# Kernel tuning notes

Hardware: AMD Instinct MI355X
Metric: run time of the kernel (lower is better)

The kernel has to match this reference:

```python
import jax, jax.numpy as jnp
import numpy as np

N = 100_000   # nodes
E = 1_600_000 # directed edges
G = 2048      # graphs in batch
NF = 78       # input node features
DIM = 32      # GIN hidden dim
L = 5         # num GIN layers
OUT = 128     # output_dim
BN_EPS = 1e-5


def setup_inputs() -> dict:
    key = jax.random.key(0)
    ks = jax.random.split(key, 8)
    s = 0.1
    return {
        "x": jax.random.normal(ks[0], (N, NF), jnp.float32),
        "edge_index": jax.random.randint(ks[1], (2, E), 0, N, jnp.int32),
        "batch": jnp.sort(jax.random.randint(ks[2], (N,), 0, G, jnp.int32)),
        "W1_0": (jax.random.normal(ks[3], (NF, DIM), jnp.float32) * s),
        "W1_rest": (jax.random.normal(ks[4], (L - 1, DIM, DIM), jnp.float32) * s),
        "b1": jnp.zeros((L, DIM), jnp.float32),
        "W2": (jax.random.normal(ks[5], (L, DIM, DIM), jnp.float32) * s),
        "b2": jnp.zeros((L, DIM), jnp.float32),
        "gamma": jnp.ones((L, DIM), jnp.float32),
        "beta": jnp.zeros((L, DIM), jnp.float32),
        "Wfc": (jax.random.normal(ks[6], (DIM, OUT), jnp.float32) * s),
        "bfc": jnp.zeros((OUT,), jnp.float32),
    }


def reference(x, edge_index, batch, W1_0, W1_rest, b1, W2, b2, gamma, beta, Wfc, bfc):
    src, dst = edge_index[0], edge_index[1]
    h = x
    for i in range(L):
        # GINConv (eps=0): h_i' = MLP(h_i + sum_{j->i} h_j)
        agg = jax.ops.segment_sum(h[src], dst, num_segments=N)  # [N, d]
        h = h + agg
        W1 = W1_0 if i == 0 else W1_rest[i - 1]
        h = jnp.maximum(h @ W1 + b1[i], 0.0) @ W2[i] + b2[i]
        # ReLU then BatchNorm1d (training mode: batch stats, biased var)
        h = jnp.maximum(h, 0.0)
        mu = h.mean(axis=0)
        var = h.var(axis=0)
        h = gamma[i] * (h - mu) * jax.lax.rsqrt(var + BN_EPS) + beta[i]
    pooled = jax.ops.segment_sum(h, batch, num_segments=G)  # global_add_pool [G, DIM]
    return jnp.maximum(pooled @ Wfc + bfc, 0.0)  # dropout is identity (eval)
```

## Files before the change

kernel.cpp:

```cpp
#include <hip/hip_runtime.h>
#include <hip/hip_fp16.h>

#define N_NODES 100000
#define N_EDGES 1600000
#define N_GRAPHS 2048
#define NFEAT 78
#define DIM 32
#define NLAYERS 5
#define OUTD 128
#define BN_EPS 1e-5f
#define NPB 32
#define NT (N_NODES / NPB)
#define NB2 ((NT + 1) / 2)
#define NBUK 391
#define BNODES 256
#define STRIDE 4608
#define EPB 4096
#define NBLK ((N_EDGES + EPB - 1) / EPB)
#define NSLOT 16
#define PSTRIDE (NSLOT * 2 * DIM)
#define OSTR (BNODES + 1)
#define WIN 4096
#define NWIN ((N_NODES + WIN - 1) / WIN)

__device__ __forceinline__ float2 up2(unsigned u) {
    __half2 h = *reinterpret_cast<__half2*>(&u);
    return __half22float2(h);
}
__device__ __forceinline__ unsigned pk2(float a, float b) {
    __half2 h = __floats2half2_rn(a, b);
    return *reinterpret_cast<unsigned*>(&h);
}

__global__ __launch_bounds__(256) void prep_kernel(
    const int* __restrict__ ei, int* __restrict__ bcnt, int* __restrict__ bdata,
    const float* __restrict__ x, const float* __restrict__ W1_0,
    unsigned short* __restrict__ y)
{
    __shared__ int cur[NBUK];
    __shared__ int gbl[NBUK];
    __shared__ float Wl[NFEAT * DIM];
    int tid = threadIdx.x;

    if (blockIdx.x < NBLK) {
        int base = blockIdx.x * EPB;
        for (int i = tid; i < NBUK; i += 256) cur[i] = 0;
        __syncthreads();

        int ew[16], eb[16];
        const int4* s4 = (const int4*)ei;
        const int4* d4 = (const int4*)(ei + N_EDGES);
#pragma unroll
        for (int c = 0; c < 4; ++c) {
            int eidx = base + c * 1024 + tid * 4;
            if (eidx < N_EDGES) {
                int4 sv = s4[eidx >> 2];
                int4 dv = d4[eidx >> 2];
                ew[c*4+0] = sv.x | ((dv.x & 255) << 17); eb[c*4+0] = dv.x >> 8;
                ew[c*4+1] = sv.y | ((dv.y & 255) << 17); eb[c*4+1] = dv.y >> 8;
                ew[c*4+2] = sv.z | ((dv.z & 255) << 17); eb[c*4+2] = dv.z >> 8;
                ew[c*4+3] = sv.w | ((dv.w & 255) << 17); eb[c*4+3] = dv.w >> 8;
            } else {
                eb[c*4+0] = eb[c*4+1] = eb[c*4+2] = eb[c*4+3] = -1;
                ew[c*4+0] = ew[c*4+1] = ew[c*4+2] = ew[c*4+3] = 0;
            }
        }
        int slot[16];
#pragma unroll
        for (int k = 0; k < 16; ++k)
            slot[k] = (eb[k] >= 0) ? atomicAdd(&cur[eb[k]], 1) : 0;
        __syncthreads();
        for (int b = tid; b < NBUK; b += 256) {
            int c = cur[b];
            gbl[b] = (c > 0) ? atomicAdd(&bcnt[b], c) : 0;
        }
        __syncthreads();
#pragma unroll
        for (int k = 0; k < 16; ++k) {
            int b = eb[k];
            if (b >= 0) {
                int pos = gbl[b] + slot[k];
                if (pos < STRIDE) bdata[b * STRIDE + pos] = ew[k];
            }
        }
    } else {
        for (int i = tid; i < NFEAT * DIM; i += 256) Wl[i] = W1_0[i];
        __syncthreads();
        int t = (blockIdx.x - NBLK) * 256 + tid;
        int row = t >> 3;
        int c0 = (t & 7) * 4;
        float a0 = 0.f, a1 = 0.f, a2 = 0.f, a3 = 0.f;
        const float* hr = x + (long)row * NFEAT;
        for (int k = 0; k < NFEAT; ++k) {
            float xv = hr[k];
            a0 = fmaf(xv, Wl[k * DIM + c0 + 0], a0);
            a1 = fmaf(xv, Wl[k * DIM + c0 + 1], a1);
            a2 = fmaf(xv, Wl[k * DIM + c0 + 2], a2);
            a3 = fmaf(xv, Wl[k * DIM + c0 + 3], a3);
        }
        ((uint2*)y)[(long)row * 8 + (t & 7)] = make_uint2(pk2(a0, a1), pk2(a2, a3));
    }
}

__global__ __launch_bounds__(256) void cfill2_kernel(
    const int* __restrict__ bcnt, const int* __restrict__ bdata,
    int* __restrict__ edge_src, int* __restrict__ offsB,
    int* __restrict__ gcursor)
{
    __shared__ int sorted[STRIDE];
    __shared__ int cnt[BNODES], off[BNODES], cur[BNODES];
    __shared__ int gbS;
    int b = blockIdx.x, tid = threadIdx.x;
    int n = min(bcnt[b], STRIDE);
    const int* slab = bdata + (long)b * STRIDE;

    if (tid == 0) gbS = atomicAdd(gcursor, n);
    if (tid < BNODES) cnt[tid] = 0;
    __syncthreads();
    int gb = gbS;
    for (int i = tid; i < n; i += 256)
        atomicAdd(&cnt[slab[i] >> 17], 1);
    __syncthreads();
    int t = tid;
    if (t < BNODES) off[t] = cnt[t];
    __syncthreads();
    for (int o = 1; o < BNODES; o <<= 1) {
        int a = (t >= o && t < BNODES) ? off[t - o] : 0;
        __syncthreads();
        if (t < BNODES) off[t] += a;
        __syncthreads();
    }
    if (t < BNODES) {
        int excl = off[t] - cnt[t];
        off[t] = excl;
        cur[t] = excl;
        offsB[b * OSTR + t] = gb + excl;
    }
    if (tid == 0) offsB[b * OSTR + BNODES] = gb + n;
    __syncthreads();
    for (int i = tid; i < n; i += 256) {
        int w = slab[i];
        int pos = atomicAdd(&cur[w >> 17], 1);
        sorted[pos] = w & 0x1FFFF;
    }
    __syncthreads();
    for (int i = tid; i < n; i += 256)
        edge_src[gb + i] = sorted[i];
}

__global__ __launch_bounds__(256) void wsort_kernel(
    const int* __restrict__ offsB, int* __restrict__ perm)
{
    __shared__ int hist[64], cur[64];
    int tid = threadIdx.x;
    int wbase = blockIdx.x * WIN;
    int wn = min(WIN, N_NODES - wbase);
    if (tid < 64) hist[tid] = 0;
    __syncthreads();
    int bins[WIN / 256];
#pragma unroll
    for (int k = 0; k < WIN / 256; ++k) {
        int i = k * 256 + tid;
        int bin = -1;
        if (i < wn) {
            int node = wbase + i;
            int ob = (node >> 8) * OSTR + (node & 255);
            bin = min(offsB[ob + 1] - offsB[ob], 63);
            atomicAdd(&hist[bin], 1);
        }
        bins[k] = bin;
    }
    __syncthreads();
    if (tid < 64) {
        int v = hist[tid];
        int s = v;
        for (int off = 1; off < 64; off <<= 1) {
            int a = __shfl_up(s, off, 64);
            if ((tid & 63) >= off) s += a;
        }
        cur[tid] = s - v;
    }
    __syncthreads();
#pragma unroll
    for (int k = 0; k < WIN / 256; ++k) {
        int bin = bins[k];
        if (bin >= 0) {
            int node = wbase + k * 256 + tid;
            int p = atomicAdd(&cur[bin], 1);
            perm[wbase + p] = node;
        }
    }
}

template<bool MM>
__global__ __launch_bounds__(256) void layer_kernel(
    const int* __restrict__ perm,
    const int* __restrict__ offsB, const int* __restrict__ edge_src,
    const unsigned short* __restrict__ zin,
    const float* __restrict__ W1g,
    const float* __restrict__ partial_prev,
    const float* __restrict__ gprev, const float* __restrict__ bprev,
    const float* __restrict__ b1v,
    const float* __restrict__ W2, const float* __restrict__ b2v,
    unsigned short* __restrict__ zout, float* __restrict__ partial)
{
    __shared__ float W1l[DIM * DIM];
    __shared__ float W2l[DIM * DIM];
    __shared__ float zs[NPB][36];
    __shared__ float b1l[DIM], b2l[DIM], cl[DIM];
    __shared__ float sscl[DIM], sshl[DIM];
    __shared__ float psum[DIM], psq[DIM];

    int tid = threadIdx.x;
    float* red = &zs[0][0];

    for (int i = tid; i < DIM * DIM; i += 256) W2l[i] = W2[i];
    if (tid < DIM) {
        b1l[tid] = b1v[tid]; b2l[tid] = b2v[tid];
        psum[tid] = 0.f; psq[tid] = 0.f;
    }
    if (MM) {
        int c = tid & 63, chunk = tid >> 6;
        float a = 0.f;
        for (int p = chunk; p < NSLOT; p += 4) a += partial_prev[p * 64 + c];
        red[tid] = a;
        __syncthreads();
        if (tid < 64) red[tid] = red[tid] + red[tid+64] + red[tid+128] + red[tid+192];
        __syncthreads();
        if (tid < DIM) {
            const float invN = 1.0f / (float)N_NODES;
            float S = red[tid], Q = red[tid + DIM];
            float mu = S * invN;
            float var = Q * invN - mu * mu;
            float sc = gprev[tid] * rsqrtf(var + BN_EPS);
            sscl[tid] = sc;
            sshl[tid] = bprev[tid] - mu * sc;
        }
        __syncthreads();
        for (int i = tid; i < DIM * DIM; i += 256) W1l[i] = sscl[i >> 5] * W1g[i];
        if (tid < DIM) {
            float cv = 0.f;
            for (int k = 0; k < DIM; ++k) cv = fmaf(sshl[k], W1g[k * DIM + tid], cv);
            cl[tid] = cv;
        }
    }
    __syncthreads();

    int ln = tid >> 3, p = tid & 7;
    int c0 = p * 4;
    const uint2* zb = (const uint2*)zin;

#pragma unroll 1
    for (int tt = 0; tt < 2; ++tt) {
        int tile = tt ? (NT - 1 - (int)blockIdx.x) : (int)blockIdx.x;
        if (tt && tile <= (int)blockIdx.x) break;

        int node = perm[tile * NPB + ln];
        int ob = (node >> 8) * OSTR + (node & 255);
        int beg = offsB[ob], end = offsB[ob + 1];
        int deg = end - beg;

        uint2 sv = zb[(long)node * 8 + p];
        float2 f;
        f = up2(sv.x); float a0 = f.x, a1 = f.y;
        f = up2(sv.y); float a2 = f.x, a3 = f.y;
        int e = beg;
        for (; e + 8 <= end; e += 8) {
            uint2 v0 = zb[(long)edge_src[e + 0] * 8 + p];
            uint2 v1 = zb[(long)edge_src[e + 1] * 8 + p];
            uint2 v2 = zb[(long)edge_src[e + 2] * 8 + p];
            uint2 v3 = zb[(long)edge_src[e + 3] * 8 + p];
            uint2 v4 = zb[(long)edge_src[e + 4] * 8 + p];
            uint2 v5 = zb[(long)edge_src[e + 5] * 8 + p];
            uint2 v6 = zb[(long)edge_src[e + 6] * 8 + p];
            uint2 v7 = zb[(long)edge_src[e + 7] * 8 + p];
            f = up2(v0.x); a0 += f.x; a1 += f.y;  f = up2(v0.y); a2 += f.x; a3 += f.y;
            f = up2(v1.x); a0 += f.x; a1 += f.y;  f = up2(v1.y); a2 += f.x; a3 += f.y;
            f = up2(v2.x); a0 += f.x; a1 += f.y;  f = up2(v2.y); a2 += f.x; a3 += f.y;
            f = up2(v3.x); a0 += f.x; a1 += f.y;  f = up2(v3.y); a2 += f.x; a3 += f.y;
            f = up2(v4.x); a0 += f.x; a1 += f.y;  f = up2(v4.y); a2 += f.x; a3 += f.y;
            f = up2(v5.x); a0 += f.x; a1 += f.y;  f = up2(v5.y); a2 += f.x; a3 += f.y;
            f = up2(v6.x); a0 += f.x; a1 += f.y;  f = up2(v6.y); a2 += f.x; a3 += f.y;
            f = up2(v7.x); a0 += f.x; a1 += f.y;  f = up2(v7.y); a2 += f.x; a3 += f.y;
        }
        for (; e < end; ++e) {
            uint2 v = zb[(long)edge_src[e] * 8 + p];
            f = up2(v.x); a0 += f.x; a1 += f.y;
            f = up2(v.y); a2 += f.x; a3 += f.y;
        }
        *(float4*)&zs[ln][c0] = make_float4(a0, a1, a2, a3);

        float t4[4];
        if (MM) {
            t4[0] = t4[1] = t4[2] = t4[3] = 0.f;
#pragma unroll
            for (int k = 0; k < DIM; ++k) {
                float zk = zs[ln][k];
                t4[0] = fmaf(zk, W1l[k * DIM + c0 + 0], t4[0]);
                t4[1] = fmaf(zk, W1l[k * DIM + c0 + 1], t4[1]);
                t4[2] = fmaf(zk, W1l[k * DIM + c0 + 2], t4[2]);
                t4[3] = fmaf(zk, W1l[k * DIM + c0 + 3], t4[3]);
            }
            float dp1 = (float)(deg + 1);
#pragma unroll
            for (int j = 0; j < 4; ++j)
                t4[j] = fmaxf(fmaf(dp1, cl[c0 + j], t4[j]) + b1l[c0 + j], 0.f);
        } else {
            t4[0] = fmaxf(a0 + b1l[c0 + 0], 0.f);
            t4[1] = fmaxf(a1 + b1l[c0 + 1], 0.f);
            t4[2] = fmaxf(a2 + b1l[c0 + 2], 0.f);
            t4[3] = fmaxf(a3 + b1l[c0 + 3], 0.f);
        }
        *(float4*)&zs[ln][c0] = make_float4(t4[0], t4[1], t4[2], t4[3]);

        float zv[4] = { b2l[c0 + 0], b2l[c0 + 1], b2l[c0 + 2], b2l[c0 + 3] };
#pragma unroll
        for (int k = 0; k < DIM; ++k) {
            float sk = zs[ln][k];
            zv[0] = fmaf(sk, W2l[k * DIM + c0 + 0], zv[0]);
            zv[1] = fmaf(sk, W2l[k * DIM + c0 + 1], zv[1]);
            zv[2] = fmaf(sk, W2l[k * DIM + c0 + 2], zv[2]);
            zv[3] = fmaf(sk, W2l[k * DIM + c0 + 3], zv[3]);
        }
#pragma unroll
        for (int j = 0; j < 4; ++j) zv[j] = fmaxf(zv[j], 0.f);
        ((uint2*)zout)[(long)node * 8 + p] =
            make_uint2(pk2(zv[0], zv[1]), pk2(zv[2], zv[3]));

        float sq[4];
#pragma unroll
        for (int j = 0; j < 4; ++j) sq[j] = zv[j] * zv[j];
#pragma unroll
        for (int off = 8; off < 64; off <<= 1) {
#pragma unroll
            for (int j = 0; j < 4; ++j) {
                zv[j] += __shfl_xor(zv[j], off, 64);
                sq[j] += __shfl_xor(sq[j], off, 64);
            }
        }
        if ((tid & 63) < 8) {
#pragma unroll
            for (int j = 0; j < 4; ++j) {
                atomicAdd(&psum[c0 + j], zv[j]);
                atomicAdd(&psq[c0 + j], sq[j]);
            }
        }
    }

    __syncthreads();
    if (tid < 2 * DIM) {
        float v = (tid < DIM) ? psum[tid] : psq[tid - DIM];
        atomicAdd(&partial[(blockIdx.x & (NSLOT - 1)) * 2 * DIM + tid], v);
    }
}

__global__ __launch_bounds__(256) void pool_kernel(
    const unsigned short* __restrict__ z, const int* __restrict__ batch,
    float* __restrict__ praw, float* __restrict__ cntg)
{
    __shared__ float acc[32][32];
    __shared__ float cntL[32];
    __shared__ int slot[32];
    __shared__ int segg[32];
    __shared__ int nsegS;
    int tid = threadIdx.x;
    for (int i = tid; i < 1024; i += 256) ((float*)acc)[i] = 0.f;
    if (tid < 32) cntL[tid] = 0.f;
    int nodeBase = blockIdx.x * 32;
    if (tid < 32) {
        int nd = nodeBase + tid;
        int gv = batch[nd];
        int flag = (tid == 0) ? 1 : (gv != batch[nd - 1]);
        unsigned long long m = __ballot(flag);
        int s = __popcll(m & ((2ull << tid) - 1ull)) - 1;
        slot[tid] = s;
        if (flag) segg[s] = gv;
        if (tid == 0) nsegS = __popcll(m);
    }
    __syncthreads();

    int ln = tid >> 3;
    int p = tid & 7;
    long node = nodeBase + ln;
    uint2 u = ((const uint2*)z)[node * 8 + p];
    int c = p * 4;
    float2 f01 = up2(u.x), f23 = up2(u.y);
    int s = slot[ln];
    atomicAdd(&acc[s][c+0], f01.x);
    atomicAdd(&acc[s][c+1], f01.y);
    atomicAdd(&acc[s][c+2], f23.x);
    atomicAdd(&acc[s][c+3], f23.y);
    if (p == 0) atomicAdd(&cntL[s], 1.f);
    __syncthreads();

    int total = nsegS * 32;
    for (int i = tid; i < total; i += 256) {
        int r = i >> 5, dd = i & 31;
        float val = acc[r][dd];
        if (val != 0.f) atomicAdd(&praw[(long)segg[r] * DIM + dd], val);
    }
    if (tid < nsegS) atomicAdd(&cntg[segg[tid]], cntL[tid]);
}

__global__ __launch_bounds__(256) void fc_kernel(
    const float* __restrict__ praw, const float* __restrict__ cntg,
    const float* __restrict__ partial4,
    const float* __restrict__ g4, const float* __restrict__ be4,
    const float* __restrict__ Wfc, const float* __restrict__ bfc,
    float* __restrict__ out)
{
    __shared__ float Wl[DIM * OUTD];
    __shared__ float red[256];
    __shared__ float sscl[DIM], sshl[DIM], dvec[OUTD];
    int tid = threadIdx.x;
    for (int i = tid; i < DIM * OUTD; i += 256) Wl[i] = Wfc[i];
    {
        int c = tid & 63, chunk = tid >> 6;
        float a = 0.f;
        for (int p = chunk; p < NSLOT; p += 4) a += partial4[p * 64 + c];
        red[tid] = a;
    }
    __syncthreads();
    if (tid < 64) red[tid] = red[tid] + red[tid+64] + red[tid+128] + red[tid+192];
    __syncthreads();
    if (tid < DIM) {
        const float invN = 1.0f / (float)N_NODES;
        float S = red[tid], Q = red[tid + DIM];
        float mu = S * invN;
        float var = Q * invN - mu * mu;
        float sc = g4[tid] * rsqrtf(var + BN_EPS);
        sscl[tid] = sc;
        sshl[tid] = be4[tid] - mu * sc;
    }
    __syncthreads();
    if (tid < OUTD) {
        float dv = 0.f;
        for (int k = 0; k < DIM; ++k) dv = fmaf(sshl[k], Wl[k * OUTD + tid], dv);
        dvec[tid] = dv;
    }
    __syncthreads();
    int t = blockIdx.x * 256 + tid;
    int g = t >> 7;
    int o = t & (OUTD - 1);
    float acc = bfc[o] + cntg[g] * dvec[o];
    const float* pr = praw + (long)g * DIM;
#pragma unroll
    for (int k = 0; k < DIM; ++k)
        acc = fmaf(sscl[k] * pr[k], Wl[k * OUTD + o], acc);
    out[t] = fmaxf(acc, 0.f);
}

extern "C" void kernel_launch(void* const* d_in, const int* in_sizes, int n_in,
                              void* d_out, int out_size, void* d_ws, size_t ws_size,
                              hipStream_t stream) {
    const float* x      = (const float*)d_in[0];
    const int*   ei     = (const int*)  d_in[1];
    const int*   batch  = (const int*)  d_in[2];
    const float* W1_0   = (const float*)d_in[3];
    const float* W1_rest= (const float*)d_in[4];
    const float* b1     = (const float*)d_in[5];
    const float* W2     = (const float*)d_in[6];
    const float* b2     = (const float*)d_in[7];
    const float* gamma  = (const float*)d_in[8];
    const float* beta   = (const float*)d_in[9];
    const float* Wfc    = (const float*)d_in[10];
    const float* bfc    = (const float*)d_in[11];
    float* out = (float*)d_out;

    int* wsi = (int*)d_ws;
    const size_t nf = (size_t)N_NODES * DIM;
    const size_t BD = (size_t)NBUK * STRIDE;
    int*   bdata  = wsi;
    unsigned short* zfpA = (unsigned short*)(wsi + BD);
    unsigned short* zfpB = zfpA + nf;
    int*   edge_src = (int*)(zfpB + nf);
    int*   offsB  = edge_src + N_EDGES;
    int*   perm   = offsB + NBUK * OSTR;
    int*   bcnt   = perm + N_NODES;
    int*   gcursor= bcnt + NBUK;
    float* praw   = (float*)(gcursor + 1);
    float* cntg   = praw + (size_t)N_GRAPHS * DIM;
    float* partial= cntg + N_GRAPHS;

    hipMemsetAsync(praw, 0,
        ((size_t)N_GRAPHS * DIM + N_GRAPHS + NLAYERS * PSTRIDE) * sizeof(float),
        stream);
    hipMemsetAsync(bcnt, 0, (size_t)(NBUK + 1) * sizeof(int), stream);

    const int grpBlocks = (N_NODES * 8) / 256;

    prep_kernel<<<NBLK + grpBlocks, 256, 0, stream>>>(
        ei, bcnt, bdata, x, W1_0, zfpA);
    cfill2_kernel<<<NBUK, 256, 0, stream>>>(
        bcnt, bdata, edge_src, offsB, gcursor);
    wsort_kernel<<<NWIN, 256, 0, stream>>>(offsB, perm);

    layer_kernel<false><<<NB2, 256, 0, stream>>>(
        perm, offsB, edge_src, zfpA, nullptr, nullptr, nullptr, nullptr,
        b1, W2, b2, zfpB, partial);

    const unsigned short* zi = zfpB;
    unsigned short* zo = zfpA;
    for (int i = 1; i < NLAYERS; ++i) {
        layer_kernel<true><<<NB2, 256, 0, stream>>>(
            perm, offsB, edge_src, zi,
            W1_rest + (size_t)(i - 1) * DIM * DIM,
            partial + (size_t)(i - 1) * PSTRIDE,
            gamma + (i - 1) * DIM, beta + (i - 1) * DIM,
            b1 + i * DIM, W2 + (size_t)i * DIM * DIM, b2 + i * DIM,
            zo, partial + (size_t)i * PSTRIDE);
        const unsigned short* tmp = zi; zi = zo; zo = (unsigned short*)tmp;
    }

    pool_kernel<<<N_NODES / 32, 256, 0, stream>>>(zi, batch, praw, cntg);
    fc_kernel<<<(N_GRAPHS * OUTD) / 256, 256, 0, stream>>>(
        praw, cntg, partial + (size_t)(NLAYERS - 1) * PSTRIDE,
        gamma + (NLAYERS - 1) * DIM, beta + (NLAYERS - 1) * DIM,
        Wfc, bfc, out);
}
```

Measured before the change: 274.6 us.

## Reorder edge lists into degree-sorted permutation order with packed offset/degree info

The degree-sort pass now also computes, per permuted position, a new edge offset and degree, and a new copy kernel rewrites the CSR source lists in permuted node order. Layer kernels read a packed int2 (begin, degree) by permuted index instead of an indirect offset lookup, and traverse edges that are contiguous across neighbouring threads. The aim is fewer dependent loads and better locality on edge index reads across the five layers. The cost is an extra, poorly coalesced per-node copy kernel, more atomics in the sort, and reuse of the bucket buffer as edge storage.

```diff
diff --git a/kernel.cpp b/kernel.cpp
--- a/kernel.cpp
+++ b/kernel.cpp
@@ -149,26 +149,32 @@
 }
 
 __global__ __launch_bounds__(256) void wsort_kernel(
-    const int* __restrict__ offsB, int* __restrict__ perm)
-{
-    __shared__ int hist[64], cur[64];
+    const int* __restrict__ offsB, int* __restrict__ perm,
+    int2* __restrict__ pinfo, int* __restrict__ obeg,
+    int* __restrict__ ecursor)
+{
+    __shared__ int hist[64], cur[64], dsum[64], dcur[64];
+    __shared__ int ebaseS;
     int tid = threadIdx.x;
     int wbase = blockIdx.x * WIN;
     int wn = min(WIN, N_NODES - wbase);
-    if (tid < 64) hist[tid] = 0;
-    __syncthreads();
-    int bins[WIN / 256];
+    if (tid < 64) { hist[tid] = 0; dsum[tid] = 0; }
+    __syncthreads();
+    int bins[WIN / 256], degs[WIN / 256], obg[WIN / 256];
 #pragma unroll
     for (int k = 0; k < WIN / 256; ++k) {
         int i = k * 256 + tid;
-        int bin = -1;
+        int bin = -1, d = 0, ob = 0;
         if (i < wn) {
             int node = wbase + i;
-            int ob = (node >> 8) * OSTR + (node & 255);
-            bin = min(offsB[ob + 1] - offsB[ob], 63);
+            int o = (node >> 8) * OSTR + (node & 255);
+            ob = offsB[o];
+            d = offsB[o + 1] - ob;
+            bin = min(d, 63);
             atomicAdd(&hist[bin], 1);
-        }
-        bins[k] = bin;
+            atomicAdd(&dsum[bin], d);
+        }
+        bins[k] = bin; degs[k] = d; obg[k] = ob;
     }
     __syncthreads();
     if (tid < 64) {
@@ -179,23 +185,47 @@
             if ((tid & 63) >= off) s += a;
         }
         cur[tid] = s - v;
-    }
-    __syncthreads();
+        int dv = dsum[tid];
+        int ds = dv;
+        for (int off = 1; off < 64; off <<= 1) {
+            int a = __shfl_up(ds, off, 64);
+            if ((tid & 63) >= off) ds += a;
+        }
+        dcur[tid] = ds - dv;
+        if (tid == 63) ebaseS = atomicAdd(ecursor, ds);
+    }
+    __syncthreads();
+    int eb = ebaseS;
 #pragma unroll
     for (int k = 0; k < WIN / 256; ++k) {
         int bin = bins[k];
         if (bin >= 0) {
             int node = wbase + k * 256 + tid;
             int p = atomicAdd(&cur[bin], 1);
+            int eo = atomicAdd(&dcur[bin], degs[k]);
             perm[wbase + p] = node;
-        }
-    }
+            pinfo[wbase + p] = make_int2(eb + eo, degs[k]);
+            obeg[wbase + p] = obg[k];
+        }
+    }
+}
+
+__global__ __launch_bounds__(256) void ecopy_kernel(
+    const int2* __restrict__ pinfo, const int* __restrict__ obeg,
+    const int* __restrict__ edge_src, int* __restrict__ edge_new)
+{
+    int i = blockIdx.x * 256 + threadIdx.x;
+    if (i >= N_NODES) return;
+    int2 bd = pinfo[i];
+    int ob = obeg[i];
+    for (int j = 0; j < bd.y; ++j)
+        edge_new[bd.x + j] = edge_src[ob + j];
 }
 
 template<bool MM>
 __global__ __launch_bounds__(256) void layer_kernel(
-    const int* __restrict__ perm,
-    const int* __restrict__ offsB, const int* __restrict__ edge_src,
+    const int* __restrict__ perm, const int2* __restrict__ pinfo,
+    const int* __restrict__ edge_new,
     const unsigned short* __restrict__ zin,
     const float* __restrict__ W1g,
     const float* __restrict__ partial_prev,
@@ -255,10 +285,10 @@
         int tile = tt ? (NT - 1 - (int)blockIdx.x) : (int)blockIdx.x;
         if (tt && tile <= (int)blockIdx.x) break;
 
-        int node = perm[tile * NPB + ln];
-        int ob = (node >> 8) * OSTR + (node & 255);
-        int beg = offsB[ob], end = offsB[ob + 1];
-        int deg = end - beg;
+        int idx = tile * NPB + ln;
+        int node = perm[idx];
+        int2 bd = pinfo[idx];
+        int beg = bd.x, deg = bd.y, end = beg + deg;
 
         uint2 sv = zb[(long)node * 8 + p];
         float2 f;
@@ -266,14 +296,14 @@
         f = up2(sv.y); float a2 = f.x, a3 = f.y;
         int e = beg;
         for (; e + 8 <= end; e += 8) {
-            uint2 v0 = zb[(long)edge_src[e + 0] * 8 + p];
-            uint2 v1 = zb[(long)edge_src[e + 1] * 8 + p];
-            uint2 v2 = zb[(long)edge_src[e + 2] * 8 + p];
-            uint2 v3 = zb[(long)edge_src[e + 3] * 8 + p];
-            uint2 v4 = zb[(long)edge_src[e + 4] * 8 + p];
-            uint2 v5 = zb[(long)edge_src[e + 5] * 8 + p];
-            uint2 v6 = zb[(long)edge_src[e + 6] * 8 + p];
-            uint2 v7 = zb[(long)edge_src[e + 7] * 8 + p];
+            uint2 v0 = zb[(long)edge_new[e + 0] * 8 + p];
+            uint2 v1 = zb[(long)edge_new[e + 1] * 8 + p];
+            uint2 v2 = zb[(long)edge_new[e + 2] * 8 + p];
+            uint2 v3 = zb[(long)edge_new[e + 3] * 8 + p];
+            uint2 v4 = zb[(long)edge_new[e + 4] * 8 + p];
+            uint2 v5 = zb[(long)edge_new[e + 5] * 8 + p];
+            uint2 v6 = zb[(long)edge_new[e + 6] * 8 + p];
+            uint2 v7 = zb[(long)edge_new[e + 7] * 8 + p];
             f = up2(v0.x); a0 += f.x; a1 += f.y;  f = up2(v0.y); a2 += f.x; a3 += f.y;
             f = up2(v1.x); a0 += f.x; a1 += f.y;  f = up2(v1.y); a2 += f.x; a3 += f.y;
             f = up2(v2.x); a0 += f.x; a1 += f.y;  f = up2(v2.y); a2 += f.x; a3 += f.y;
@@ -284,7 +314,7 @@
             f = up2(v7.x); a0 += f.x; a1 += f.y;  f = up2(v7.y); a2 += f.x; a3 += f.y;
         }
         for (; e < end; ++e) {
-            uint2 v = zb[(long)edge_src[e] * 8 + p];
+            uint2 v = zb[(long)edge_new[e] * 8 + p];
             f = up2(v.x); a0 += f.x; a1 += f.y;
             f = up2(v.y); a2 += f.x; a3 += f.y;
         }
@@ -471,21 +501,25 @@
     const size_t nf = (size_t)N_NODES * DIM;
     const size_t BD = (size_t)NBUK * STRIDE;
     int*   bdata  = wsi;
+    int*   edge_new = bdata;
     unsigned short* zfpA = (unsigned short*)(wsi + BD);
     unsigned short* zfpB = zfpA + nf;
     int*   edge_src = (int*)(zfpB + nf);
-    int*   offsB  = edge_src + N_EDGES;
+    int2*  pinfo  = (int2*)(edge_src + N_EDGES);
+    int*   obeg   = (int*)(pinfo + N_NODES);
+    int*   offsB  = obeg + N_NODES;
     int*   perm   = offsB + NBUK * OSTR;
     int*   bcnt   = perm + N_NODES;
     int*   gcursor= bcnt + NBUK;
-    float* praw   = (float*)(gcursor + 1);
+    int*   ecursor= gcursor + 1;
+    float* praw   = (float*)(ecursor + 1);
     float* cntg   = praw + (size_t)N_GRAPHS * DIM;
     float* partial= cntg + N_GRAPHS;
 
     hipMemsetAsync(praw, 0,
         ((size_t)N_GRAPHS * DIM + N_GRAPHS + NLAYERS * PSTRIDE) * sizeof(float),
         stream);
-    hipMemsetAsync(bcnt, 0, (size_t)(NBUK + 1) * sizeof(int), stream);
+    hipMemsetAsync(bcnt, 0, (size_t)(NBUK + 2) * sizeof(int), stream);
 
     const int grpBlocks = (N_NODES * 8) / 256;
 
@@ -493,17 +527,19 @@
         ei, bcnt, bdata, x, W1_0, zfpA);
     cfill2_kernel<<<NBUK, 256, 0, stream>>>(
         bcnt, bdata, edge_src, offsB, gcursor);
-    wsort_kernel<<<NWIN, 256, 0, stream>>>(offsB, perm);
+    wsort_kernel<<<NWIN, 256, 0, stream>>>(offsB, perm, pinfo, obeg, ecursor);
+    ecopy_kernel<<<(N_NODES + 255) / 256, 256, 0, stream>>>(
+        pinfo, obeg, edge_src, edge_new);
 
     layer_kernel<false><<<NB2, 256, 0, stream>>>(
-        perm, offsB, edge_src, zfpA, nullptr, nullptr, nullptr, nullptr,
+        perm, pinfo, edge_new, zfpA, nullptr, nullptr, nullptr, nullptr,
         b1, W2, b2, zfpB, partial);
 
     const unsigned short* zi = zfpB;
     unsigned short* zo = zfpA;
     for (int i = 1; i < NLAYERS; ++i) {
         layer_kernel<true><<<NB2, 256, 0, stream>>>(
-            perm, offsB, edge_src, zi,
+            perm, pinfo, edge_new, zi,
             W1_rest + (size_t)(i - 1) * DIM * DIM,
             partial + (size_t)(i - 1) * PSTRIDE,
             gamma + (i - 1) * DIM, beta + (i - 1) * DIM,
```

Result: slower. 280.8 us (+2.3%).
